# Kernel optimization log

Hardware: AMD Instinct MI355X
Metric: run time of the kernel (lower is better)

The kernel has to match this reference:

```python
import jax, jax.numpy as jnp
import numpy as np
import math

NUM_HEADS = 16


def setup_inputs() -> dict:
    key = jax.random.key(0)
    ks = jax.random.split(key, 5)
    L, B, E = 2048, 2, 1024
    scale = 1.0 / math.sqrt(E)
    return {
        "query": jax.random.normal(ks[0], (L, B, E), jnp.float32),
        "key": jax.random.normal(ks[1], (L, B, E), jnp.float32),
        "value": jax.random.normal(ks[2], (L, B, E), jnp.float32),
        "in_proj_weight": jax.random.normal(ks[3], (3 * E, E), jnp.float32) * scale,
        "in_proj_bias": jnp.zeros((3 * E,), jnp.float32),
        "out_w": jax.random.normal(ks[4], (E, E), jnp.float32) * scale,
        "out_b": jnp.zeros((E,), jnp.float32),
    }


def reference(query, key, value, in_proj_weight, in_proj_bias, out_w, out_b):
    L, Bz, E = query.shape
    S = key.shape[0]
    H = NUM_HEADS
    hd = E // H
    # in-projection: chunk packed weight into q/k/v parts (same math as torch chunk)
    w_q, w_k, w_v = jnp.split(in_proj_weight, 3, axis=0)
    b_q, b_k, b_v = jnp.split(in_proj_bias, 3, axis=0)
    q = query @ w_q.T + b_q            # (L, B, E)
    k = key @ w_k.T + b_k              # (S, B, E)
    v = value @ w_v.T + b_v            # (S, B, E)
    # (L, B*H, hd) -> (B*H, L, hd)
    q = q.reshape(L, Bz * H, hd).transpose(1, 0, 2) / math.sqrt(hd)
    k = k.reshape(S, Bz * H, hd).transpose(1, 0, 2)
    v = v.reshape(S, Bz * H, hd).transpose(1, 0, 2)
    # sigmoid attention (non-softmax), full (B*H, L, S) matrix as in original
    attn = jax.nn.sigmoid(jnp.einsum("bld,bsd->bls", q, k))
    denom = attn.sum(axis=-1, keepdims=True) + 1e-4
    out = jnp.einsum("bls,bsd->bld", attn / denom, v)  # (B*H, L, hd)
    out = out.transpose(1, 0, 2).reshape(L, Bz, E)
    out = out @ out_w.T + out_b
    avg_weights = attn.reshape(Bz, H, L, S).sum(axis=1) / H
    return out, avg_weights
```

## Files before the change

### kernel.cpp

```cpp
#include <hip/hip_runtime.h>
#include <stdint.h>


#define L_SEQ 2048
#define NBATCH 2
#define EMB 1024
#define NHEAD 16
#define HD 64
#define MROWS 4096

typedef __bf16 bf16x8 __attribute__((ext_vector_type(8)));
typedef float f32x4 __attribute__((ext_vector_type(4)));
typedef float f32x16 __attribute__((ext_vector_type(16)));

__device__ __forceinline__ unsigned short f2bf(float f) {
  union { float f; uint32_t u; } v; v.f = f;
  uint32_t u = v.u;
  u += 0x7fffu + ((u >> 16) & 1u);
  return (unsigned short)(u >> 16);
}

__device__ __forceinline__ unsigned short f2bf_fast(float f) {
  union { float f; uint32_t u; } v; v.f = f;
  return (unsigned short)((v.u + 0x8000u) >> 16);
}

__device__ __forceinline__ void gl_lds16(const void* gptr, void* ldsptr) {
  const uint32_t* g = reinterpret_cast<const uint32_t*>(gptr);
  auto* l = reinterpret_cast<__attribute__((address_space(3))) uint32_t*>(
      reinterpret_cast<uintptr_t>(ldsptr));
  __builtin_amdgcn_global_load_lds(g, l, 16, 0, 0);
}

__device__ __forceinline__ f32x4 mfma16(bf16x8 a, bf16x8 b, f32x4 c) {
  return __builtin_amdgcn_mfma_f32_16x16x32_bf16(a, b, c, 0, 0, 0);
}

__device__ __forceinline__ f32x16 mfma32(bf16x8 a, bf16x8 b, f32x16 c) {
  return __builtin_amdgcn_mfma_f32_32x32x16_bf16(a, b, c, 0, 0, 0);
}

__device__ __forceinline__ float fast_sigmoid(float x) {
  float e = __expf(-x);
  return __builtin_amdgcn_rcpf(1.0f + e);
}

__global__ __launch_bounds__(256) void k_convert(
    const float* __restrict__ qin, const float* __restrict__ kin,
    const float* __restrict__ vin, const float* __restrict__ win,
    const float* __restrict__ wo,
    unsigned short* __restrict__ Xq, unsigned short* __restrict__ Xk,
    unsigned short* __restrict__ Xv, unsigned short* __restrict__ Wb,
    unsigned short* __restrict__ Wob) {
  const int row = blockIdx.x;
  const int t = threadIdx.x;
  const float* src;
  unsigned short* dst;
  int srow;
  size_t drow;
  if (row < 3 * MROWS) {
    const int which = row >> 12;
    const int m = row & (MROWS - 1);
    const int b = m >> 11, l = m & (L_SEQ - 1);
    srow = l * NBATCH + b;
    drow = (size_t)m;
    src = which == 0 ? qin : (which == 1 ? kin : vin);
    dst = which == 0 ? Xq : (which == 1 ? Xk : Xv);
  } else if (row < 3 * MROWS + 3072) {
    srow = row - 3 * MROWS; drow = (size_t)srow; src = win; dst = Wb;
  } else {
    srow = row - (3 * MROWS + 3072); drow = (size_t)srow; src = wo; dst = Wob;
  }
  const float4 vv = *(const float4*)(src + (size_t)srow * EMB + t * 4);
  ushort4 o;
  o.x = f2bf(vv.x); o.y = f2bf(vv.y); o.z = f2bf(vv.z); o.w = f2bf(vv.w);
  *(ushort4*)(dst + drow * EMB + t * 4) = o;
}

__device__ __forceinline__ void gemm_core(
    const unsigned short* __restrict__ A, const unsigned short* __restrict__ Bm,
    int m0, int n0, unsigned short* sA, unsigned short* sB, f32x4 acc[4][4]) {
  const int tid = threadIdx.x;
  const int wave = tid >> 6;
  const int lane = tid & 63;
  const int quad = lane >> 4;
  const int l16 = lane & 15;
  const int wm = (wave >> 1) * 64;
  const int wn = (wave & 1) * 64;
  const int srow = lane >> 2;
  const int scol = lane & 3;

  for (int mi = 0; mi < 4; ++mi)
    for (int ni = 0; ni < 4; ++ni)
      acc[mi][ni] = (f32x4){0.f, 0.f, 0.f, 0.f};

  for (int k0 = 0; k0 < EMB; k0 += 32) {
    __syncthreads();
    for (int i = 0; i < 2; ++i) {
      const int p = wave * 2 + i;
      const int r = p * 16 + srow;
      const int c = scol ^ ((r >> 1) & 3);
      gl_lds16(A + (size_t)(m0 + r) * EMB + k0 + c * 8, sA + p * 512);
      gl_lds16(Bm + (size_t)(n0 + r) * EMB + k0 + c * 8, sB + p * 512);
    }
    __syncthreads();
    bf16x8 af[4], bfr[4];
    for (int mi = 0; mi < 4; ++mi) {
      const int r = wm + mi * 16 + l16;
      const int cp = quad ^ ((r >> 1) & 3);
      af[mi] = *(const bf16x8*)(sA + r * 32 + cp * 8);
    }
    for (int ni = 0; ni < 4; ++ni) {
      const int r = wn + ni * 16 + l16;
      const int cp = quad ^ ((r >> 1) & 3);
      bfr[ni] = *(const bf16x8*)(sB + r * 32 + cp * 8);
    }
    for (int mi = 0; mi < 4; ++mi)
      for (int ni = 0; ni < 4; ++ni)
        acc[mi][ni] = mfma16(af[mi], bfr[ni], acc[mi][ni]);
  }
}

__global__ __launch_bounds__(256) void k_inproj(
    const unsigned short* __restrict__ Xq, const unsigned short* __restrict__ Xk,
    const unsigned short* __restrict__ Xv, const unsigned short* __restrict__ Wb,
    const float* __restrict__ bias,
    unsigned short* __restrict__ qb, unsigned short* __restrict__ kb,
    unsigned short* __restrict__ vb) {
  __shared__ __attribute__((aligned(16))) unsigned short sA[128 * 32];
  __shared__ __attribute__((aligned(16))) unsigned short sB[128 * 32];
  __shared__ __attribute__((aligned(16))) unsigned short sT[128 * 128];
  const int z = blockIdx.z;
  const unsigned short* A = z == 0 ? Xq : (z == 1 ? Xk : Xv);
  const int n0 = blockIdx.x * 128, m0 = blockIdx.y * 128;
  f32x4 acc[4][4];
  gemm_core(A, Wb + (size_t)z * EMB * EMB, m0, n0, sA, sB, acc);

  const int tid = threadIdx.x, wave = tid >> 6, lane = tid & 63;
  const int quad = lane >> 4, l16 = lane & 15;
  const int wm = (wave >> 1) * 64, wn = (wave & 1) * 64;
  const int bb = m0 >> 11, lbase = m0 & (L_SEQ - 1);
  const int lane8 = tid & 7, rowid = tid >> 3;

  if (z == 2) {
    for (int ni = 0; ni < 4; ++ni) {
      const int n = wn + ni * 16 + l16;
      const float bv = bias[2 * EMB + n0 + n];
      const int x = (n & 15) << 1;
      for (int mi = 0; mi < 4; ++mi) {
        const int mchunk = ((wm + mi * 16) >> 2) + quad;
        const int slot = mchunk ^ x;
        ushort4 pk;
        pk.x = f2bf(acc[mi][ni][0] + bv);
        pk.y = f2bf(acc[mi][ni][1] + bv);
        pk.z = f2bf(acc[mi][ni][2] + bv);
        pk.w = f2bf(acc[mi][ni][3] + bv);
        *(ushort4*)(sT + (size_t)n * 128 + slot * 4) = pk;
      }
    }
    __syncthreads();
    for (int p = 0; p < 8; ++p) {
      const int row = rowid + p * 32;
      const int n = row >> 1, hf = row & 1;
      const int x = (n & 15) << 1;
      const int c2 = hf * 16 + lane8 * 2;
      const int slot = c2 ^ x;
      uint4 vd = *(const uint4*)(sT + (size_t)n * 128 + slot * 4);
      const int ng = n0 + n;
      const int h = ng >> 6, d = ng & 63;
      unsigned short* dst =
          vb + ((size_t)(bb * NHEAD + h) * HD + d) * L_SEQ + lbase + hf * 64;
      *(uint4*)(dst + lane8 * 8) = vd;
    }
  } else {
    const float scale = (z == 0) ? 0.125f : 1.0f;
    unsigned short* dstp = (z == 0) ? qb : kb;
    for (int ni = 0; ni < 4; ++ni) {
      const int n = wn + ni * 16 + l16;
      const float bv = bias[z * EMB + n0 + n];
      for (int mi = 0; mi < 4; ++mi) {
        for (int r = 0; r < 4; ++r) {
          const int m = wm + mi * 16 + quad * 4 + r;
          const int g = (m >> 2) & 7;
          sT[(size_t)m * 128 + (n ^ (g << 4))] =
              f2bf((acc[mi][ni][r] + bv) * scale);
        }
      }
    }
    __syncthreads();
    for (int p = 0; p < 8; ++p) {
      const int row = rowid + p * 32;
      const int l = row >> 1, hf = row & 1;
      const int g2 = ((l >> 2) & 7) << 1;
      const int c = hf * 8 + lane8;
      const int slot = c ^ g2;
      uint4 vd = *(const uint4*)(sT + (size_t)l * 128 + slot * 8);
      const int ng = n0 + c * 8;
      const int h = ng >> 6, d = ng & 63;
      unsigned short* dst =
          dstp + ((size_t)(bb * NHEAD + h) * L_SEQ + lbase + l) * HD + d;
      *(uint4*)dst = vd;
    }
  }
}

__global__ __launch_bounds__(512) void k_attn(
    const unsigned short* __restrict__ qb, const unsigned short* __restrict__ kb,
    const unsigned short* __restrict__ vb, unsigned short* __restrict__ oh) {
  __shared__ __attribute__((aligned(16))) unsigned short sQ[128 * 64];
  __shared__ __attribute__((aligned(16))) unsigned short sK[64 * 64];
  __shared__ __attribute__((aligned(16))) unsigned short sV[64 * 64];
  __shared__ __attribute__((aligned(16))) unsigned short sP[128 * 72];

  const int bh = blockIdx.x;
  const int b = bh >> 4, h = bh & 15;
  const int l0 = blockIdx.y * 128;
  const unsigned short* qg = qb + ((size_t)bh * L_SEQ + l0) * HD;
  const unsigned short* kg = kb + (size_t)bh * L_SEQ * HD;
  const unsigned short* vg = vb + (size_t)bh * HD * L_SEQ;

  const int tid = threadIdx.x, wave = tid >> 6, lane = tid & 63;
  const int quad = lane >> 4, l16 = lane & 15;
  const int sr8 = lane >> 3, sc8 = lane & 7;
  const int sh = (wave >> 2) * 32;
  const int lq = (wave & 3) * 32;

  for (int i = 0; i < 2; ++i) {
    const int p = wave * 2 + i;
    const int r = p * 8 + sr8;
    const int c = sc8 ^ (r & 7);
    gl_lds16(qg + (size_t)r * HD + c * 8, sQ + p * 512);
  }

  f32x4 oacc[4];
  for (int ni = 0; ni < 4; ++ni) oacc[ni] = (f32x4){0.f, 0.f, 0.f, 0.f};
  f32x4 dacc = (f32x4){0.f, 0.f, 0.f, 0.f};

  bf16x8 ones;
  for (int j = 0; j < 8; ++j) ones[j] = (__bf16)1.0f;

  for (int s0 = 0; s0 < L_SEQ; s0 += 64) {
    __syncthreads();
    if (wave < 4) {
      for (int i = 0; i < 2; ++i) {
        const int p = wave * 2 + i;
        const int r = p * 8 + sr8;
        const int c = sc8 ^ (r & 7);
        gl_lds16(kg + (size_t)(s0 + r) * HD + c * 8, sK + p * 512);
      }
    } else {
      for (int i = 0; i < 2; ++i) {
        const int p = (wave - 4) * 2 + i;
        const int r = p * 8 + sr8;
        const int c = sc8 ^ (r & 7);
        gl_lds16(vg + (size_t)r * L_SEQ + s0 + c * 8, sV + p * 512);
      }
    }
    __syncthreads();

    f32x4 st[2][2];
    for (int smi = 0; smi < 2; ++smi)
      for (int lni = 0; lni < 2; ++lni) st[smi][lni] = (f32x4){0.f, 0.f, 0.f, 0.f};
    for (int kk = 0; kk < HD; kk += 32) {
      bf16x8 a[2], bq[2];
      for (int smi = 0; smi < 2; ++smi) {
        const int r = sh + smi * 16 + l16;
        const int c = ((kk >> 3) + quad) ^ (r & 7);
        a[smi] = *(const bf16x8*)(sK + r * 64 + c * 8);
      }
      for (int lni = 0; lni < 2; ++lni) {
        const int r = lq + lni * 16 + l16;
        const int c = ((kk >> 3) + quad) ^ (r & 7);
        bq[lni] = *(const bf16x8*)(sQ + r * 64 + c * 8);
      }
      for (int smi = 0; smi < 2; ++smi)
        for (int lni = 0; lni < 2; ++lni)
          st[smi][lni] = mfma16(a[smi], bq[lni], st[smi][lni]);
    }

    for (int lni = 0; lni < 2; ++lni) {
      const int lrow = lq + lni * 16 + l16;
      for (int smi = 0; smi < 2; ++smi) {
        uint32_t u[4];
        for (int r = 0; r < 4; ++r) {
          union { float f; uint32_t i; } cv;
          cv.f = fast_sigmoid(st[smi][lni][r]);
          u[r] = cv.i + 0x8000u;
        }
        uint2 pk;
        pk.x = __builtin_amdgcn_perm(u[1], u[0], 0x07060302u);
        pk.y = __builtin_amdgcn_perm(u[3], u[2], 0x07060302u);
        *(uint2*)(sP + (size_t)lrow * 72 + sh + smi * 16 + quad * 4) = pk;
      }
    }
    __syncthreads();

    const int lr = wave * 16 + l16;
    for (int kk = 0; kk < 64; kk += 32) {
      bf16x8 ap = *(const bf16x8*)(sP + (size_t)lr * 72 + kk + quad * 8);
      for (int ni = 0; ni < 4; ++ni) {
        const int rd = ni * 16 + l16;
        const int c = ((kk >> 3) + quad) ^ (rd & 7);
        bf16x8 bv4 = *(const bf16x8*)(sV + rd * 64 + c * 8);
        oacc[ni] = mfma16(ap, bv4, oacc[ni]);
      }
      dacc = mfma16(ap, ones, dacc);
    }
  }

  for (int r = 0; r < 4; ++r) {
    const int lrow = l0 + wave * 16 + quad * 4 + r;
    const float rden = __builtin_amdgcn_rcpf(dacc[r] + 1e-4f);
    unsigned short* dst = oh + ((size_t)(b * L_SEQ + lrow)) * EMB + h * HD;
    for (int ni = 0; ni < 4; ++ni)
      dst[ni * 16 + l16] = f2bf_fast(oacc[ni][r] * rden);
  }
}

__global__ __launch_bounds__(512) void k_avg(
    const unsigned short* __restrict__ qb, const unsigned short* __restrict__ kb,
    float* __restrict__ avg) {
  __shared__ __attribute__((aligned(16))) unsigned short sQ[2][128 * 64];
  __shared__ __attribute__((aligned(16))) unsigned short sK[2][128 * 64];
  const int ss0 = blockIdx.x * 128, l0 = blockIdx.y * 128, b = blockIdx.z;
  const int tid = threadIdx.x, wave = tid >> 6, lane = tid & 63;
  const int l32 = lane & 31, lh = lane >> 5;
  const int sr8 = lane >> 3, sc8 = lane & 7;
  const int mt = wave & 3;
  const int ntg = (wave >> 2) * 2;

  const unsigned short* qg0 = qb + ((size_t)(b * NHEAD) * L_SEQ + l0) * HD;
  const unsigned short* kg0 = kb + ((size_t)(b * NHEAD) * L_SEQ + ss0) * HD;
  const size_t hstride = (size_t)L_SEQ * HD;

  for (int i = 0; i < 2; ++i) {
    const int p = wave * 2 + i;
    const int r = p * 8 + sr8;
    const int c = sc8 ^ (r & 7);
    gl_lds16(qg0 + (size_t)r * HD + c * 8, sQ[0] + p * 512);
    gl_lds16(kg0 + (size_t)r * HD + c * 8, sK[0] + p * 512);
  }

  f32x16 av[2];
  for (int t = 0; t < 2; ++t)
    for (int i = 0; i < 16; ++i) av[t][i] = 0.f;

  for (int h = 0; h < NHEAD; ++h) {
    __syncthreads();
    const int cur = h & 1;
    if (h < NHEAD - 1) {
      const int nxt = cur ^ 1;
      const unsigned short* qg = qg0 + (size_t)(h + 1) * hstride;
      const unsigned short* kg = kg0 + (size_t)(h + 1) * hstride;
      for (int i = 0; i < 2; ++i) {
        const int p = wave * 2 + i;
        const int r = p * 8 + sr8;
        const int c = sc8 ^ (r & 7);
        gl_lds16(qg + (size_t)r * HD + c * 8, sQ[nxt] + p * 512);
        gl_lds16(kg + (size_t)r * HD + c * 8, sK[nxt] + p * 512);
      }
    }

    f32x16 scr[2];
    for (int t = 0; t < 2; ++t)
      for (int i = 0; i < 16; ++i) scr[t][i] = 0.f;
    const int qrow = mt * 32 + l32;
    for (int kk = 0; kk < 4; ++kk) {
      const int cq = (kk * 2 + lh) ^ (qrow & 7);
      bf16x8 aq = *(const bf16x8*)(sQ[cur] + qrow * 64 + cq * 8);
      for (int t = 0; t < 2; ++t) {
        const int krow = (ntg + t) * 32 + l32;
        const int ck = (kk * 2 + lh) ^ (krow & 7);
        bf16x8 bk = *(const bf16x8*)(sK[cur] + krow * 64 + ck * 8);
        scr[t] = mfma32(aq, bk, scr[t]);
      }
    }
    for (int t = 0; t < 2; ++t)
      for (int r = 0; r < 16; ++r)
        av[t][r] += fast_sigmoid(scr[t][r]);
  }

  for (int t = 0; t < 2; ++t) {
    for (int r = 0; r < 16; ++r) {
      const int l = l0 + mt * 32 + (r & 3) + 8 * (r >> 2) + 4 * lh;
      const int s = ss0 + (ntg + t) * 32 + l32;
      avg[((size_t)b * L_SEQ + l) * L_SEQ + s] = av[t][r] * 0.0625f;
    }
  }
}

__global__ __launch_bounds__(256) void k_outproj(
    const unsigned short* __restrict__ OH, const unsigned short* __restrict__ Wob,
    const float* __restrict__ ob, float* __restrict__ out) {
  __shared__ __attribute__((aligned(16))) unsigned short sA[128 * 32];
  __shared__ __attribute__((aligned(16))) unsigned short sB[128 * 32];
  const int n0 = blockIdx.x * 128, m0 = blockIdx.y * 128;
  f32x4 acc[4][4];
  gemm_core(OH, Wob, m0, n0, sA, sB, acc);

  const int tid = threadIdx.x, wave = tid >> 6, lane = tid & 63;
  const int quad = lane >> 4, l16 = lane & 15;
  const int wm = (wave >> 1) * 64, wn = (wave & 1) * 64;
  for (int ni = 0; ni < 4; ++ni) {
    const int n = n0 + wn + ni * 16 + l16;
    const float bv = ob[n];
    for (int mi = 0; mi < 4; ++mi) {
      for (int r = 0; r < 4; ++r) {
        const int m = m0 + wm + mi * 16 + quad * 4 + r;
        const int b = m >> 11, l = m & (L_SEQ - 1);
        out[((size_t)l * NBATCH + b) * EMB + n] = acc[mi][ni][r] + bv;
      }
    }
  }
}

extern "C" void kernel_launch(void* const* d_in, const int* in_sizes, int n_in,
                              void* d_out, int out_size, void* d_ws, size_t ws_size,
                              hipStream_t stream) {
  (void)in_sizes; (void)n_in; (void)out_size;
  const float* qin = (const float*)d_in[0];
  const float* kin = (const float*)d_in[1];
  const float* vin = (const float*)d_in[2];
  const float* w   = (const float*)d_in[3];
  const float* bias = (const float*)d_in[4];
  const float* wo  = (const float*)d_in[5];
  const float* ob  = (const float*)d_in[6];
  float* out = (float*)d_out;

  unsigned short* Xq  = (unsigned short*)d_ws;
  unsigned short* Xk  = Xq + (size_t)MROWS * EMB;
  unsigned short* Xv  = Xk + (size_t)MROWS * EMB;
  unsigned short* Wb  = Xv + (size_t)MROWS * EMB;
  unsigned short* Wob = Wb + (size_t)3 * EMB * EMB;
  unsigned short* qbuf = Wob + (size_t)EMB * EMB;
  unsigned short* kbuf = qbuf + (size_t)MROWS * EMB;
  unsigned short* vbuf = kbuf + (size_t)MROWS * EMB;
  unsigned short* ohb  = vbuf + (size_t)MROWS * EMB;
  const size_t need = ((size_t)MROWS * EMB * 7 + (size_t)4 * EMB * EMB) * 2;
  if (ws_size < need) return;

  k_convert<<<16384, 256, 0, stream>>>(qin, kin, vin, w, wo, Xq, Xk, Xv, Wb, Wob);
  k_inproj<<<dim3(8, 32, 3), 256, 0, stream>>>(Xq, Xk, Xv, Wb, bias, qbuf, kbuf, vbuf);
  k_attn<<<dim3(32, 16), 512, 0, stream>>>(qbuf, kbuf, vbuf, ohb);
  k_avg<<<dim3(16, 16, 2), 512, 0, stream>>>(qbuf, kbuf, out + (size_t)MROWS * EMB);
  k_outproj<<<dim3(8, 32), 256, 0, stream>>>(ohb, Wob, ob, out);
}
```

Measured before the change: 284.0 us.

## Double-buffer LDS in GEMMs and attention, keep sigmoid probs in registers

The projection GEMM core now double-buffers its A/B tiles in LDS so the next K-slice loads while the current one is computed, which removes one barrier per step. The attention kernel double-buffers K/V tiles and switches to 32x32 MFMA. It also feeds the sigmoid scores straight into the PV MFMA through ds_bpermute lane exchange rather than an LDS round-trip, and splits the S dimension across two wave groups whose partial outputs and denominators are reduced through LDS at the end. The shared-memory arrays are unified into single buffers. The cost is more LDS per block, which may lower occupancy, plus extra epilogue reduction work.

```diff
diff --git a/kernel.cpp b/kernel.cpp
--- a/kernel.cpp
+++ b/kernel.cpp
@@ -77,9 +77,9 @@
   *(ushort4*)(dst + drow * EMB + t * 4) = o;
 }
 
-__device__ __forceinline__ void gemm_core(
+__device__ __forceinline__ void gemm_core_db(
     const unsigned short* __restrict__ A, const unsigned short* __restrict__ Bm,
-    int m0, int n0, unsigned short* sA, unsigned short* sB, f32x4 acc[4][4]) {
+    int m0, int n0, unsigned short* smem, f32x4 acc[4][4]) {
   const int tid = threadIdx.x;
   const int wave = tid >> 6;
   const int lane = tid & 63;
@@ -94,30 +94,46 @@
     for (int ni = 0; ni < 4; ++ni)
       acc[mi][ni] = (f32x4){0.f, 0.f, 0.f, 0.f};
 
+  for (int i = 0; i < 2; ++i) {
+    const int p = wave * 2 + i;
+    const int r = p * 16 + srow;
+    const int c = scol ^ ((r >> 1) & 3);
+    gl_lds16(A + (size_t)(m0 + r) * EMB + c * 8, smem + p * 512);
+    gl_lds16(Bm + (size_t)(n0 + r) * EMB + c * 8, smem + 8192 + p * 512);
+  }
+
+  int buf = 0;
   for (int k0 = 0; k0 < EMB; k0 += 32) {
     __syncthreads();
-    for (int i = 0; i < 2; ++i) {
-      const int p = wave * 2 + i;
-      const int r = p * 16 + srow;
-      const int c = scol ^ ((r >> 1) & 3);
-      gl_lds16(A + (size_t)(m0 + r) * EMB + k0 + c * 8, sA + p * 512);
-      gl_lds16(Bm + (size_t)(n0 + r) * EMB + k0 + c * 8, sB + p * 512);
-    }
-    __syncthreads();
+    if (k0 + 32 < EMB) {
+      const int nb = buf ^ 1;
+      unsigned short* dA = smem + nb * 4096;
+      unsigned short* dB = smem + 8192 + nb * 4096;
+      for (int i = 0; i < 2; ++i) {
+        const int p = wave * 2 + i;
+        const int r = p * 16 + srow;
+        const int c = scol ^ ((r >> 1) & 3);
+        gl_lds16(A + (size_t)(m0 + r) * EMB + k0 + 32 + c * 8, dA + p * 512);
+        gl_lds16(Bm + (size_t)(n0 + r) * EMB + k0 + 32 + c * 8, dB + p * 512);
+      }
+    }
+    const unsigned short* rA = smem + buf * 4096;
+    const unsigned short* rB = smem + 8192 + buf * 4096;
     bf16x8 af[4], bfr[4];
     for (int mi = 0; mi < 4; ++mi) {
       const int r = wm + mi * 16 + l16;
       const int cp = quad ^ ((r >> 1) & 3);
-      af[mi] = *(const bf16x8*)(sA + r * 32 + cp * 8);
+      af[mi] = *(const bf16x8*)(rA + r * 32 + cp * 8);
     }
     for (int ni = 0; ni < 4; ++ni) {
       const int r = wn + ni * 16 + l16;
       const int cp = quad ^ ((r >> 1) & 3);
-      bfr[ni] = *(const bf16x8*)(sB + r * 32 + cp * 8);
+      bfr[ni] = *(const bf16x8*)(rB + r * 32 + cp * 8);
     }
     for (int mi = 0; mi < 4; ++mi)
       for (int ni = 0; ni < 4; ++ni)
         acc[mi][ni] = mfma16(af[mi], bfr[ni], acc[mi][ni]);
+    buf ^= 1;
   }
 }
 
@@ -127,14 +143,14 @@
     const float* __restrict__ bias,
     unsigned short* __restrict__ qb, unsigned short* __restrict__ kb,
     unsigned short* __restrict__ vb) {
-  __shared__ __attribute__((aligned(16))) unsigned short sA[128 * 32];
-  __shared__ __attribute__((aligned(16))) unsigned short sB[128 * 32];
-  __shared__ __attribute__((aligned(16))) unsigned short sT[128 * 128];
+  __shared__ __attribute__((aligned(16))) unsigned short smem[16384];
+  unsigned short* sT = smem;
   const int z = blockIdx.z;
   const unsigned short* A = z == 0 ? Xq : (z == 1 ? Xk : Xv);
   const int n0 = blockIdx.x * 128, m0 = blockIdx.y * 128;
   f32x4 acc[4][4];
-  gemm_core(A, Wb + (size_t)z * EMB * EMB, m0, n0, sA, sB, acc);
+  gemm_core_db(A, Wb + (size_t)z * EMB * EMB, m0, n0, smem, acc);
+  __syncthreads();
 
   const int tid = threadIdx.x, wave = tid >> 6, lane = tid & 63;
   const int quad = lane >> 4, l16 = lane & 15;
@@ -207,10 +223,9 @@
 __global__ __launch_bounds__(512) void k_attn(
     const unsigned short* __restrict__ qb, const unsigned short* __restrict__ kb,
     const unsigned short* __restrict__ vb, unsigned short* __restrict__ oh) {
-  __shared__ __attribute__((aligned(16))) unsigned short sQ[128 * 64];
-  __shared__ __attribute__((aligned(16))) unsigned short sK[64 * 64];
-  __shared__ __attribute__((aligned(16))) unsigned short sV[64 * 64];
-  __shared__ __attribute__((aligned(16))) unsigned short sP[128 * 72];
+  __shared__ __attribute__((aligned(16))) unsigned short smem[25088];
+  unsigned short* sQ = smem;
+  float* sDen = (float*)(smem + 24576);
 
   const int bh = blockIdx.x;
   const int b = bh >> 4, h = bh & 15;
@@ -220,10 +235,10 @@
   const unsigned short* vg = vb + (size_t)bh * HD * L_SEQ;
 
   const int tid = threadIdx.x, wave = tid >> 6, lane = tid & 63;
-  const int quad = lane >> 4, l16 = lane & 15;
+  const int l32 = lane & 31, lh = lane >> 5;
   const int sr8 = lane >> 3, sc8 = lane & 7;
-  const int sh = (wave >> 2) * 32;
-  const int lq = (wave & 3) * 32;
+  const int lq = wave & 3, sh = wave >> 2;
+  const int pidx = (lane ^ 32) << 2;
 
   for (int i = 0; i < 2; ++i) {
     const int p = wave * 2 + i;
@@ -231,97 +246,133 @@
     const int c = sc8 ^ (r & 7);
     gl_lds16(qg + (size_t)r * HD + c * 8, sQ + p * 512);
   }
-
-  f32x4 oacc[4];
-  for (int ni = 0; ni < 4; ++ni) oacc[ni] = (f32x4){0.f, 0.f, 0.f, 0.f};
-  f32x4 dacc = (f32x4){0.f, 0.f, 0.f, 0.f};
-
-  bf16x8 ones;
-  for (int j = 0; j < 8; ++j) ones[j] = (__bf16)1.0f;
-
-  for (int s0 = 0; s0 < L_SEQ; s0 += 64) {
+  if (wave < 4) {
+    for (int i = 0; i < 2; ++i) {
+      const int p = wave * 2 + i;
+      const int r = p * 8 + sr8;
+      const int c = sc8 ^ (r & 7);
+      gl_lds16(kg + (size_t)r * HD + c * 8, smem + 8192 + p * 512);
+    }
+  } else {
+    for (int i = 0; i < 2; ++i) {
+      const int p = (wave - 4) * 2 + i;
+      const int r = p * 8 + sr8;
+      const int c = sc8 ^ (r & 7);
+      gl_lds16(vg + (size_t)r * L_SEQ + c * 8, smem + 16384 + p * 512);
+    }
+  }
+
+  f32x16 oacc[2];
+  for (int dh = 0; dh < 2; ++dh)
+    for (int i = 0; i < 16; ++i) oacc[dh][i] = 0.f;
+  float dp = 0.f;
+
+  int buf = 0;
+  const int rs = sh * 32 + l32;
+  const int rl = lq * 32 + l32;
+  for (int it = 0; it < 32; ++it) {
     __syncthreads();
-    if (wave < 4) {
-      for (int i = 0; i < 2; ++i) {
-        const int p = wave * 2 + i;
-        const int r = p * 8 + sr8;
-        const int c = sc8 ^ (r & 7);
-        gl_lds16(kg + (size_t)(s0 + r) * HD + c * 8, sK + p * 512);
-      }
-    } else {
-      for (int i = 0; i < 2; ++i) {
-        const int p = (wave - 4) * 2 + i;
-        const int r = p * 8 + sr8;
-        const int c = sc8 ^ (r & 7);
-        gl_lds16(vg + (size_t)r * L_SEQ + s0 + c * 8, sV + p * 512);
-      }
-    }
-    __syncthreads();
-
-    f32x4 st[2][2];
-    for (int smi = 0; smi < 2; ++smi)
-      for (int lni = 0; lni < 2; ++lni) st[smi][lni] = (f32x4){0.f, 0.f, 0.f, 0.f};
-    for (int kk = 0; kk < HD; kk += 32) {
-      bf16x8 a[2], bq[2];
-      for (int smi = 0; smi < 2; ++smi) {
-        const int r = sh + smi * 16 + l16;
-        const int c = ((kk >> 3) + quad) ^ (r & 7);
-        a[smi] = *(const bf16x8*)(sK + r * 64 + c * 8);
-      }
-      for (int lni = 0; lni < 2; ++lni) {
-        const int r = lq + lni * 16 + l16;
-        const int c = ((kk >> 3) + quad) ^ (r & 7);
-        bq[lni] = *(const bf16x8*)(sQ + r * 64 + c * 8);
-      }
-      for (int smi = 0; smi < 2; ++smi)
-        for (int lni = 0; lni < 2; ++lni)
-          st[smi][lni] = mfma16(a[smi], bq[lni], st[smi][lni]);
-    }
-
-    for (int lni = 0; lni < 2; ++lni) {
-      const int lrow = lq + lni * 16 + l16;
-      for (int smi = 0; smi < 2; ++smi) {
-        uint32_t u[4];
-        for (int r = 0; r < 4; ++r) {
-          union { float f; uint32_t i; } cv;
-          cv.f = fast_sigmoid(st[smi][lni][r]);
-          u[r] = cv.i + 0x8000u;
+    if (it < 31) {
+      const int nb = buf ^ 1;
+      const int s1 = (it + 1) * 64;
+      if (wave < 4) {
+        unsigned short* dK = smem + 8192 + nb * 4096;
+        for (int i = 0; i < 2; ++i) {
+          const int p = wave * 2 + i;
+          const int r = p * 8 + sr8;
+          const int c = sc8 ^ (r & 7);
+          gl_lds16(kg + (size_t)(s1 + r) * HD + c * 8, dK + p * 512);
         }
-        uint2 pk;
-        pk.x = __builtin_amdgcn_perm(u[1], u[0], 0x07060302u);
-        pk.y = __builtin_amdgcn_perm(u[3], u[2], 0x07060302u);
-        *(uint2*)(sP + (size_t)lrow * 72 + sh + smi * 16 + quad * 4) = pk;
-      }
-    }
-    __syncthreads();
-
-    const int lr = wave * 16 + l16;
-    for (int kk = 0; kk < 64; kk += 32) {
-      bf16x8 ap = *(const bf16x8*)(sP + (size_t)lr * 72 + kk + quad * 8);
-      for (int ni = 0; ni < 4; ++ni) {
-        const int rd = ni * 16 + l16;
-        const int c = ((kk >> 3) + quad) ^ (rd & 7);
-        bf16x8 bv4 = *(const bf16x8*)(sV + rd * 64 + c * 8);
-        oacc[ni] = mfma16(ap, bv4, oacc[ni]);
-      }
-      dacc = mfma16(ap, ones, dacc);
-    }
-  }
-
-  for (int r = 0; r < 4; ++r) {
-    const int lrow = l0 + wave * 16 + quad * 4 + r;
-    const float rden = __builtin_amdgcn_rcpf(dacc[r] + 1e-4f);
-    unsigned short* dst = oh + ((size_t)(b * L_SEQ + lrow)) * EMB + h * HD;
-    for (int ni = 0; ni < 4; ++ni)
-      dst[ni * 16 + l16] = f2bf_fast(oacc[ni][r] * rden);
+      } else {
+        unsigned short* dV = smem + 16384 + nb * 4096;
+        for (int i = 0; i < 2; ++i) {
+          const int p = (wave - 4) * 2 + i;
+          const int r = p * 8 + sr8;
+          const int c = sc8 ^ (r & 7);
+          gl_lds16(vg + (size_t)r * L_SEQ + s1 + c * 8, dV + p * 512);
+        }
+      }
+    }
+
+    f32x16 st;
+    for (int i = 0; i < 16; ++i) st[i] = 0.f;
+    const unsigned short* sKb = smem + 8192 + buf * 4096;
+    #pragma unroll
+    for (int kk = 0; kk < 4; ++kk) {
+      const int ca = (2 * kk + lh) ^ (rs & 7);
+      const int cb = (2 * kk + lh) ^ (rl & 7);
+      bf16x8 a = *(const bf16x8*)(sKb + rs * 64 + ca * 8);
+      bf16x8 q = *(const bf16x8*)(sQ + rl * 64 + cb * 8);
+      st = mfma32(a, q, st);
+    }
+
+    uint32_t pd[8];
+    #pragma unroll
+    for (int g = 0; g < 8; ++g) {
+      const int rg = 4 * (g >> 1) + 2 * (g & 1);
+      const float pa = fast_sigmoid(st[rg]);
+      const float pb = fast_sigmoid(st[rg + 1]);
+      dp += pa + pb;
+      union { float f; uint32_t u; } ca, cb;
+      ca.f = pa; cb.f = pb;
+      pd[g] = __builtin_amdgcn_perm(cb.u + 0x8000u, ca.u + 0x8000u, 0x07060302u);
+    }
+
+    const unsigned short* sVb = smem + 16384 + buf * 4096;
+    #pragma unroll
+    for (int j = 0; j < 2; ++j) {
+      const uint32_t s0 = lh ? pd[4 * j + 0] : pd[4 * j + 2];
+      const uint32_t s1 = lh ? pd[4 * j + 1] : pd[4 * j + 3];
+      const uint32_t r0 = (uint32_t)__builtin_amdgcn_ds_bpermute(pidx, (int)s0);
+      const uint32_t r1 = (uint32_t)__builtin_amdgcn_ds_bpermute(pidx, (int)s1);
+      union { uint32_t w[4]; bf16x8 v; } af;
+      af.w[0] = lh ? r0 : pd[4 * j + 0];
+      af.w[1] = lh ? r1 : pd[4 * j + 1];
+      af.w[2] = lh ? pd[4 * j + 2] : r0;
+      af.w[3] = lh ? pd[4 * j + 3] : r1;
+      const int c8 = 4 * sh + 2 * j + lh;
+      #pragma unroll
+      for (int dh = 0; dh < 2; ++dh) {
+        const int rd = dh * 32 + l32;
+        bf16x8 bv = *(const bf16x8*)(sVb + rd * 64 + ((c8 ^ (rd & 7)) * 8));
+        oacc[dh] = mfma32(af.v, bv, oacc[dh]);
+      }
+    }
+    buf ^= 1;
+  }
+
+  __syncthreads();
+  float dp2 = dp + __shfl_xor(dp, 32, 64);
+  if (lh == 0) sDen[sh * 128 + lq * 32 + l32] = dp2;
+  float* scr = (float*)smem;
+  if (sh == 1) {
+    float* w = scr + lq * 2304 + lane * 36;
+    #pragma unroll
+    for (int dh = 0; dh < 2; ++dh)
+      for (int r = 0; r < 16; ++r) w[dh * 16 + r] = oacc[dh][r];
+  }
+  __syncthreads();
+  if (sh == 0) {
+    const float* rs2 = scr + lq * 2304 + lane * 36;
+    #pragma unroll
+    for (int dh = 0; dh < 2; ++dh)
+      for (int r = 0; r < 16; ++r) oacc[dh][r] += rs2[dh * 16 + r];
+    #pragma unroll
+    for (int r = 0; r < 16; ++r) {
+      const int l = lq * 32 + (r & 3) + 8 * (r >> 2) + 4 * lh;
+      const float rden =
+          __builtin_amdgcn_rcpf(sDen[l] + sDen[128 + l] + 1e-4f);
+      unsigned short* dst = oh + ((size_t)(b * L_SEQ + l0 + l)) * EMB + h * HD;
+      dst[l32] = f2bf_fast(oacc[0][r] * rden);
+      dst[32 + l32] = f2bf_fast(oacc[1][r] * rden);
+    }
   }
 }
 
 __global__ __launch_bounds__(512) void k_avg(
     const unsigned short* __restrict__ qb, const unsigned short* __restrict__ kb,
     float* __restrict__ avg) {
-  __shared__ __attribute__((aligned(16))) unsigned short sQ[2][128 * 64];
-  __shared__ __attribute__((aligned(16))) unsigned short sK[2][128 * 64];
+  __shared__ __attribute__((aligned(16))) unsigned short smem[32768];
   const int ss0 = blockIdx.x * 128, l0 = blockIdx.y * 128, b = blockIdx.z;
   const int tid = threadIdx.x, wave = tid >> 6, lane = tid & 63;
   const int l32 = lane & 31, lh = lane >> 5;
@@ -337,8 +388,8 @@
     const int p = wave * 2 + i;
     const int r = p * 8 + sr8;
     const int c = sc8 ^ (r & 7);
-    gl_lds16(qg0 + (size_t)r * HD + c * 8, sQ[0] + p * 512);
-    gl_lds16(kg0 + (size_t)r * HD + c * 8, sK[0] + p * 512);
+    gl_lds16(qg0 + (size_t)r * HD + c * 8, smem + p * 512);
+    gl_lds16(kg0 + (size_t)r * HD + c * 8, smem + 16384 + p * 512);
   }
 
   f32x16 av[2];
@@ -352,26 +403,30 @@
       const int nxt = cur ^ 1;
       const unsigned short* qg = qg0 + (size_t)(h + 1) * hstride;
       const unsigned short* kg = kg0 + (size_t)(h + 1) * hstride;
+      unsigned short* dQ = smem + nxt * 8192;
+      unsigned short* dK = smem + 16384 + nxt * 8192;
       for (int i = 0; i < 2; ++i) {
         const int p = wave * 2 + i;
         const int r = p * 8 + sr8;
         const int c = sc8 ^ (r & 7);
-        gl_lds16(qg + (size_t)r * HD + c * 8, sQ[nxt] + p * 512);
-        gl_lds16(kg + (size_t)r * HD + c * 8, sK[nxt] + p * 512);
-      }
-    }
-
+        gl_lds16(qg + (size_t)r * HD + c * 8, dQ + p * 512);
+        gl_lds16(kg + (size_t)r * HD + c * 8, dK + p * 512);
+      }
+    }
+
+    const unsigned short* sQb = smem + cur * 8192;
+    const unsigned short* sKb = smem + 16384 + cur * 8192;
     f32x16 scr[2];
     for (int t = 0; t < 2; ++t)
       for (int i = 0; i < 16; ++i) scr[t][i] = 0.f;
     const int qrow = mt * 32 + l32;
     for (int kk = 0; kk < 4; ++kk) {
       const int cq = (kk * 2 + lh) ^ (qrow & 7);
-      bf16x8 aq = *(const bf16x8*)(sQ[cur] + qrow * 64 + cq * 8);
+      bf16x8 aq = *(const bf16x8*)(sQb + qrow * 64 + cq * 8);
       for (int t = 0; t < 2; ++t) {
         const int krow = (ntg + t) * 32 + l32;
         const int ck = (kk * 2 + lh) ^ (krow & 7);
-        bf16x8 bk = *(const bf16x8*)(sK[cur] + krow * 64 + ck * 8);
+        bf16x8 bk = *(const bf16x8*)(sKb + krow * 64 + ck * 8);
         scr[t] = mfma32(aq, bk, scr[t]);
       }
     }
@@ -392,11 +447,10 @@
 __global__ __launch_bounds__(256) void k_outproj(
     const unsigned short* __restrict__ OH, const unsigned short* __restrict__ Wob,
     const float* __restrict__ ob, float* __restrict__ out) {
-  __shared__ __attribute__((aligned(16))) unsigned short sA[128 * 32];
-  __shared__ __attribute__((aligned(16))) unsigned short sB[128 * 32];
+  __shared__ __attribute__((aligned(16))) unsigned short smem[16384];
   const int n0 = blockIdx.x * 128, m0 = blockIdx.y * 128;
   f32x4 acc[4][4];
-  gemm_core(OH, Wob, m0, n0, sA, sB, acc);
+  gemm_core_db(OH, Wob, m0, n0, smem, acc);
 
   const int tid = threadIdx.x, wave = tid >> 6, lane = tid & 63;
   const int quad = lane >> 4, l16 = lane & 15;
```

Result: faster. 276.2 us (-2.8%).
